# Kernel tuning notes

Hardware: AMD Instinct MI355X
Metric: run time of the kernel (lower is better)

Reference implementation:

```python
import jax, jax.numpy as jnp
import numpy as np

NUM_FRAMES = 24
FRAME_SIZE = 8          # heads per frame; attention_probs.shape[0] = NUM_FRAMES*FRAME_SIZE
DIM_X = 32
DIM_Y = 32
SEQ = 300
STRENGTHEN_SCALE = 0.125
WEAKEN_SCALE = 0.918
INJECTION_SCALE = 1.0
KERNEL_DIVISION = 3.0
LEN_PROMPT = 8          # 'A basketball player missing a three-point shot'
TRAILING = 100
# token_inds=[2,3] union trailing range (9..108); order irrelevant (uniform write)
TOKEN_INDS = np.array(sorted(set([2, 3]) | set(range(LEN_PROMPT + 1, LEN_PROMPT + TRAILING + 1))), dtype=np.int32)
_LEFTS = [0.05, 0.0717, 0.0935, 0.1152, 0.137, 0.1587, 0.1804, 0.2022, 0.2239, 0.2457,
          0.2674, 0.2891, 0.3109, 0.3326, 0.3543, 0.3761, 0.3978, 0.4196, 0.4413, 0.463,
          0.4848, 0.5065, 0.5283, 0.55]
# [top, left, bottom, right] ratios per frame (matches init_kwargs bbox_per_frame)
BBOX_PER_FRAME = [(0.25, l, 0.75, round(l + 0.3, 4)) for l in _LEFTS]


def _bbox_px(ratios, dim_x, dim_y):
    top = int(dim_y * ratios[0]); left = int(dim_x * ratios[1])
    bottom = int(dim_y * ratios[2]); right = int(dim_x * ratios[3])
    return top, left, bottom, right


def _gauss_patch(h, w):
    # torch.linspace(0, h, h): h points, endpoint inclusive; mx=int(h/2), sx=h/3
    x = jnp.linspace(0.0, float(h), h)[:, None]
    y = jnp.linspace(0.0, float(w), w)[None, :]
    sx, sy = h / KERNEL_DIVISION, w / KERNEL_DIVISION
    g = jnp.exp(-(((x - h // 2) ** 2) / (2.0 * sx * sx) + ((y - w // 2) ** 2) / (2.0 * sy * sy)))
    return g / g.max()  # 1/(2*pi*sx*sy) prefactor cancels under max-normalization


def _forward(attention_probs, dim_x, dim_y):
    F = NUM_FRAMES
    fs = attention_probs.shape[0] // F
    seq = attention_probs.shape[-1]
    max_val = attention_probs.max()
    scale = max_val * INJECTION_SCALE
    # strengthen map is identical across heads-within-frame and across selected tokens:
    # build a compact [F, dim_y, dim_x] map instead of the full 4D zeros_like tensor.
    wm = jnp.zeros((F, dim_y, dim_x), attention_probs.dtype)
    for i, r in enumerate(BBOX_PER_FRAME):  # fixed small frame count, trace-time loop
        t, l, b, rt = _bbox_px(r, dim_x, dim_y)
        wm = wm.at[i, t:b, l:rt].set(_gauss_patch(b - t, rt - l).astype(attention_probs.dtype) * scale)
    inds = TOKEN_INDS
    ap5 = attention_probs.reshape(F, fs, dim_y, dim_x, seq)
    sel = ap5[..., inds]                     # [F, fs, dy, dx, T]
    wmb = wm[:, None, :, :, None]            # broadcast over heads & tokens
    weaken = jnp.where(wmb == 0, WEAKEN_SCALE, 1.0).astype(attention_probs.dtype)
    new_sel = sel * weaken + STRENGTHEN_SCALE * wmb
    out = ap5.at[..., inds].set(new_sel)
    return out.reshape(attention_probs.shape)


def setup_inputs() -> dict:
    key = jax.random.key(0)
    ap = jax.random.uniform(key, (NUM_FRAMES * FRAME_SIZE, DIM_Y, DIM_X, SEQ), dtype=jnp.float32)
    return {"attention_probs": ap, "dim_x": DIM_X, "dim_y": DIM_Y}


def reference(attention_probs, dim_x, dim_y):
    return _forward(attention_probs, dim_x, dim_y)
```

## Files before the change

### kernel.cpp

```cpp
#include <hip/hip_runtime.h>

#define SEQ        300
#define V4         (SEQ / 4)
#define NROWS      (192 * 32 * 32)
#define N4         (NROWS * V4)
#define NFRAMES    24
#define MAXBLOCKS  1024

__constant__ int c_left[NFRAMES]  = {1,2,2,3,4,5,5,6,7,7,8,9,9,10,11,12,12,13,14,14,15,16,16,17};
__constant__ int c_width[NFRAMES] = {10,9,10,10,9,9,10,10,9,10,10,9,10,10,9,9,10,10,9,10,10,9,10,10};

__device__ __forceinline__ float wave_max64(float v) {
    #pragma unroll
    for (int off = 32; off > 0; off >>= 1)
        v = fmaxf(v, __shfl_down(v, off, 64));
    return v;
}

__global__ void kmax(const float4* __restrict__ in, float* __restrict__ bmax) {
    float m = 0.0f;
    int stride = gridDim.x * blockDim.x;
    for (int i = blockIdx.x * blockDim.x + threadIdx.x; i < N4; i += stride) {
        float4 v = in[i];
        m = fmaxf(fmaxf(m, v.x), fmaxf(fmaxf(v.y, v.z), v.w));
    }
    m = wave_max64(m);
    __shared__ float sw[4];
    int lane = threadIdx.x & 63, wv = threadIdx.x >> 6;
    if (lane == 0) sw[wv] = m;
    __syncthreads();
    if (threadIdx.x == 0) {
        float r = fmaxf(fmaxf(sw[0], sw[1]), fmaxf(sw[2], sw[3]));
        bmax[blockIdx.x] = r;
    }
}

__global__ void kwm(const float* __restrict__ bmax, float* __restrict__ wm) {
    __shared__ float patch[16 * 10];
    __shared__ float sw[4];
    __shared__ float s_scale, s_gmax;
    const int f = blockIdx.x;
    const int tid = threadIdx.x;

    float m = 0.0f;
    for (int i = tid; i < MAXBLOCKS; i += 256) m = fmaxf(m, bmax[i]);
    m = wave_max64(m);
    if ((tid & 63) == 0) sw[tid >> 6] = m;
    __syncthreads();
    if (tid == 0) s_scale = fmaxf(fmaxf(sw[0], sw[1]), fmaxf(sw[2], sw[3]));

    const int w = c_width[f], l = c_left[f];
    if (tid < 16 * w) {
        int i = tid / w, j = tid - i * w;
        float x = (float)i * (16.0f / 15.0f);
        float y = (float)j * ((float)w / (float)(w - 1));
        float dx = x - 8.0f;
        float dy = y - (float)(w / 2);
        float sx = 16.0f / 3.0f;
        float sy = (float)w / 3.0f;
        patch[tid] = expf(-(dx * dx / (2.0f * sx * sx) + dy * dy / (2.0f * sy * sy)));
    }
    __syncthreads();
    if (tid == 0) {
        float g = 0.0f;
        for (int k = 0; k < 16 * w; k++) g = fmaxf(g, patch[k]);
        s_gmax = g;
    }
    __syncthreads();
    const float mul = s_scale / s_gmax;
    for (int p = tid; p < 1024; p += 256) {
        int yy = p >> 5, xx = p & 31;
        float v = 0.0f;
        if (yy >= 8 && yy < 24 && xx >= l && xx < l + w)
            v = patch[(yy - 8) * w + (xx - l)] * mul;
        wm[f * 1024 + p] = v;
    }
}

__global__ void kapply(const float4* __restrict__ in, float4* __restrict__ out,
                       const float* __restrict__ wm) {
    int idx = blockIdx.x * 256 + threadIdx.x;
    int row = idx / V4;
    int c   = idx - row * V4;
    float wmv = wm[((row >> 13) << 10) | (row & 1023)];
    float4 v = in[idx];
    float weaken = (wmv == 0.0f) ? 0.918f : 1.0f;
    float add = 0.125f * wmv;
    int s0 = c * 4;
    float r[4] = {v.x, v.y, v.z, v.w};
    #pragma unroll
    for (int k = 0; k < 4; k++) {
        int s = s0 + k;
        bool tok = (s == 2) | (s == 3) | ((s >= 9) & (s <= 108));
        if (tok) r[k] = r[k] * weaken + add;
    }
    out[idx] = make_float4(r[0], r[1], r[2], r[3]);
}

extern "C" void kernel_launch(void* const* d_in, const int* in_sizes, int n_in,
                              void* d_out, int out_size, void* d_ws, size_t ws_size,
                              hipStream_t stream) {
    const float* ap = (const float*)d_in[0];
    float* out = (float*)d_out;
    float* ws  = (float*)d_ws;
    float* bmax = ws;
    float* wm   = ws + 1024;

    kmax<<<MAXBLOCKS, 256, 0, stream>>>((const float4*)ap, bmax);
    kwm<<<NFRAMES, 256, 0, stream>>>(bmax, wm);
    kapply<<<N4 / 256, 256, 0, stream>>>((const float4*)ap, (float4*)out, wm);
}
```

Before: 427.0 us.

## Fuse max reduction with weaken pass, then add strengthen term only inside bboxes

The max reduction is merged into a single streaming pass that also writes the output, applying the 0.918 weaken factor to selected tokens outside each frame's bbox. A small follow-up kernel then adds the scaled Gaussian term in place, only for bbox pixels and selected tokens. This drops the second full read of the input, cutting traffic from roughly three passes to two. The costs are a much larger per-block max buffer (N4/256 entries) that kwm must reduce, and scattered, uncoalesced read-modify-write updates in the inject kernel.

After: 424.9 us. About the same (-0.5%).

```diff
diff --git a/kernel.cpp b/kernel.cpp
--- a/kernel.cpp
+++ b/kernel.cpp
@@ -5,7 +5,7 @@
 #define NROWS      (192 * 32 * 32)
 #define N4         (NROWS * V4)
 #define NFRAMES    24
-#define MAXBLOCKS  1024
+#define P1BLOCKS   (N4 / 256)
 
 __constant__ int c_left[NFRAMES]  = {1,2,2,3,4,5,5,6,7,7,8,9,9,10,11,12,12,13,14,14,15,16,16,17};
 __constant__ int c_width[NFRAMES] = {10,9,10,10,9,9,10,10,9,10,10,9,10,10,9,9,10,10,9,10,10,9,10,10};
@@ -17,22 +17,39 @@
     return v;
 }
 
-__global__ void kmax(const float4* __restrict__ in, float* __restrict__ bmax) {
-    float m = 0.0f;
-    int stride = gridDim.x * blockDim.x;
-    for (int i = blockIdx.x * blockDim.x + threadIdx.x; i < N4; i += stride) {
-        float4 v = in[i];
-        m = fmaxf(fmaxf(m, v.x), fmaxf(fmaxf(v.y, v.z), v.w));
+__global__ void kphase1(const float4* __restrict__ in, float4* __restrict__ out,
+                        float* __restrict__ bmax) {
+    int idx = blockIdx.x * 256 + threadIdx.x;
+    int row = idx / V4;
+    int c   = idx - row * V4;
+    int f   = row >> 13;
+    int yy  = (row >> 5) & 31;
+    int xx  = row & 31;
+    int l   = c_left[f];
+    bool inB = (yy >= 8) & (yy < 24) & (xx >= l) & (xx < l + c_width[f]);
+
+    float4 v = in[idx];
+    float m = fmaxf(fmaxf(v.x, v.y), fmaxf(v.z, v.w));
+
+    float r[4] = {v.x, v.y, v.z, v.w};
+    if (!inB) {
+        int s0 = c * 4;
+        #pragma unroll
+        for (int k = 0; k < 4; k++) {
+            int s = s0 + k;
+            bool tok = (s == 2) | (s == 3) | ((s >= 9) & (s <= 108));
+            if (tok) r[k] *= 0.918f;
+        }
     }
+    out[idx] = make_float4(r[0], r[1], r[2], r[3]);
+
     m = wave_max64(m);
     __shared__ float sw[4];
     int lane = threadIdx.x & 63, wv = threadIdx.x >> 6;
     if (lane == 0) sw[wv] = m;
     __syncthreads();
-    if (threadIdx.x == 0) {
-        float r = fmaxf(fmaxf(sw[0], sw[1]), fmaxf(sw[2], sw[3]));
-        bmax[blockIdx.x] = r;
-    }
+    if (threadIdx.x == 0)
+        bmax[blockIdx.x] = fmaxf(fmaxf(sw[0], sw[1]), fmaxf(sw[2], sw[3]));
 }
 
 __global__ void kwm(const float* __restrict__ bmax, float* __restrict__ wm) {
@@ -43,7 +60,7 @@
     const int tid = threadIdx.x;
 
     float m = 0.0f;
-    for (int i = tid; i < MAXBLOCKS; i += 256) m = fmaxf(m, bmax[i]);
+    for (int i = tid; i < P1BLOCKS; i += 256) m = fmaxf(m, bmax[i]);
     m = wave_max64(m);
     if ((tid & 63) == 0) sw[tid >> 6] = m;
     __syncthreads();
@@ -77,24 +94,22 @@
     }
 }
 
-__global__ void kapply(const float4* __restrict__ in, float4* __restrict__ out,
-                       const float* __restrict__ wm) {
-    int idx = blockIdx.x * 256 + threadIdx.x;
-    int row = idx / V4;
-    int c   = idx - row * V4;
-    float wmv = wm[((row >> 13) << 10) | (row & 1023)];
-    float4 v = in[idx];
-    float weaken = (wmv == 0.0f) ? 0.918f : 1.0f;
-    float add = 0.125f * wmv;
-    int s0 = c * 4;
-    float r[4] = {v.x, v.y, v.z, v.w};
-    #pragma unroll
-    for (int k = 0; k < 4; k++) {
-        int s = s0 + k;
-        bool tok = (s == 2) | (s == 3) | ((s >= 9) & (s <= 108));
-        if (tok) r[k] = r[k] * weaken + add;
+__global__ void kinject(float* __restrict__ out, const float* __restrict__ wm) {
+    const int b  = blockIdx.x;
+    const int f  = b >> 7;
+    const int fs = (b >> 4) & 7;
+    const int yy = (b & 15) + 8;
+    const int l  = c_left[f], w = c_width[f];
+    const int r0 = ((f * 8 + fs) * 32 + yy) * 32;
+    const int total = w * 102;
+
+    for (int t = threadIdx.x; t < total; t += 256) {
+        int xi = t / 102;
+        int si = t - xi * 102;
+        int s  = (si < 2) ? (si + 2) : (si + 7);
+        float add = 0.125f * wm[f * 1024 + yy * 32 + l + xi];
+        out[(r0 + l + xi) * SEQ + s] += add;
     }
-    out[idx] = make_float4(r[0], r[1], r[2], r[3]);
 }
 
 extern "C" void kernel_launch(void* const* d_in, const int* in_sizes, int n_in,
@@ -104,9 +119,9 @@
     float* out = (float*)d_out;
     float* ws  = (float*)d_ws;
     float* bmax = ws;
-    float* wm   = ws + 1024;
+    float* wm   = ws + P1BLOCKS;
 
-    kmax<<<MAXBLOCKS, 256, 0, stream>>>((const float4*)ap, bmax);
+    kphase1<<<P1BLOCKS, 256, 0, stream>>>((const float4*)ap, (float4*)out, bmax);
     kwm<<<NFRAMES, 256, 0, stream>>>(bmax, wm);
-    kapply<<<N4 / 256, 256, 0, stream>>>((const float4*)ap, (float4*)out, wm);
+    kinject<<<24 * 8 * 16, 256, 0, stream>>>(out, wm);
 }
```
